# Kernel optimization log

Measured on AMD Instinct MI355X. Metric: run time of the kernel, lower is better.

The kernel has to match this reference:

```python
import jax, jax.numpy as jnp
import numpy as np

N = 50000          # nodes
E = 1_600_000      # edges (avg degree 32)
IN = 128           # in_channels
H1, C1 = 4, 8      # conv1: heads=4, out=8 -> concat 32
OUT = 64           # out_channels (conv2, heads=1)
NEG_SLOPE = 0.2    # PyG GATConv default LeakyReLU slope


def _gat_layer(x, edge_index, W, att_src, att_dst, bias, heads, out_ch):
    """PyG-style GATConv (concat=True, add_self_loops=True).
    x: [N, F_in], edge_index: [2, E], W: [F_in, heads*out_ch],
    att_src/att_dst: [heads, out_ch], bias: [heads*out_ch].
    """
    n = x.shape[0]
    loops = jnp.arange(n)
    src = jnp.concatenate([edge_index[0], loops])  # message source j
    dst = jnp.concatenate([edge_index[1], loops])  # aggregation target i

    h = (x @ W).reshape(n, heads, out_ch)                 # [N, H, C]
    a_src = jnp.sum(h * att_src, axis=-1)                 # [N, H]
    a_dst = jnp.sum(h * att_dst, axis=-1)                 # [N, H]

    logits = jax.nn.leaky_relu(a_src[src] + a_dst[dst], NEG_SLOPE)  # [E', H]
    # segment softmax over incoming edges of each destination node
    m = jax.ops.segment_max(logits, dst, num_segments=n)            # [N, H]
    e = jnp.exp(logits - m[dst])
    s = jax.ops.segment_sum(e, dst, num_segments=n)                 # [N, H]
    alpha = e / (s[dst] + 1e-16)                                    # [E', H]

    msg = h[src] * alpha[..., None]                                 # [E', H, C]
    out = jax.ops.segment_sum(msg, dst, num_segments=n)             # [N, H, C]
    return out.reshape(n, heads * out_ch) + bias


def setup_inputs() -> dict:
    key = jax.random.key(0)
    ks = jax.random.split(key, 10)
    g = 0.1
    x = jax.random.normal(ks[0], (N, IN), jnp.float32)
    edge_index = jax.random.randint(ks[1], (2, E), 0, N, dtype=jnp.int64)
    W1 = jax.random.normal(ks[2], (IN, H1 * C1), jnp.float32) * g
    att_src1 = jax.random.normal(ks[3], (H1, C1), jnp.float32) * g
    att_dst1 = jax.random.normal(ks[4], (H1, C1), jnp.float32) * g
    b1 = jnp.zeros((H1 * C1,), jnp.float32)
    W2 = jax.random.normal(ks[5], (H1 * C1, OUT), jnp.float32) * g
    att_src2 = jax.random.normal(ks[6], (1, OUT), jnp.float32) * g
    att_dst2 = jax.random.normal(ks[7], (1, OUT), jnp.float32) * g
    b2 = jnp.zeros((OUT,), jnp.float32)
    return {"x": x, "edge_index": edge_index,
            "W1": W1, "att_src1": att_src1, "att_dst1": att_dst1, "b1": b1,
            "W2": W2, "att_src2": att_src2, "att_dst2": att_dst2, "b2": b2}


def reference(x, edge_index, W1, att_src1, att_dst1, b1, W2, att_src2, att_dst2, b2):
    h = _gat_layer(x, edge_index, W1, att_src1, att_dst1, b1, H1, C1)   # [N, 32]
    h = jax.nn.relu(h)
    out = _gat_layer(h, edge_index, W2, att_src2, att_dst2, b2, 1, OUT)  # [N, 64]
    return out
```

## Files before the change

### kernel.cpp

```cpp
#include <hip/hip_runtime.h>
#include <hip/hip_bf16.h>

#define IN_CH 128
#define H1C1  32
#define NH1   4
#define OUTC  64
#define NEG   0.2f
#define RPAD  16
#define BSH   6
#define BSZ   64
#define NBMAX 1024
#define CHUNK 4096
#define CAP   3072
#define PCAP  4096

typedef __hip_bfloat16 bf16;
typedef unsigned int u32;
typedef unsigned short u16;

__device__ __forceinline__ u16 f2bf_bits(float f) {
  bf16 v = __float2bfloat16(f);
  return *(u16*)&v;
}
__device__ __forceinline__ float bflo(u32 g) { return __uint_as_float(g << 16); }
__device__ __forceinline__ float bfhi(u32 g) { return __uint_as_float(g & 0xFFFF0000u); }

__global__ __launch_bounds__(256) void k_bin_tr(
    const int* __restrict__ ei, int* __restrict__ bucket_fill,
    u32* __restrict__ data, int E, int n, int nb, int nA,
    const float* __restrict__ x, const float* __restrict__ W1,
    const float* __restrict__ as1, const float* __restrict__ ad1,
    u16* __restrict__ h1b, float* __restrict__ a_src, float* __restrict__ a_dst) {
  __shared__ __align__(16) char smem[28672];
  int t = threadIdx.x;
  if ((int)blockIdx.x < nA) {
    int* cnt   = (int*)smem;
    int* lbase = cnt + NBMAX;
    int* gbase = lbase + NBMAX;
    u32* staged = (u32*)(gbase + NBMAX);
    int lane = t & 63, wid = t >> 6;
    for (int b = t; b < nb; b += 256) cnt[b] = 0;
    __syncthreads();
    long base = (long)blockIdx.x * CHUNK;
    long totE = (long)E + n;
    u32 pk[CHUNK / 256];
    int bk[CHUNK / 256];
#pragma unroll
    for (int i = 0; i < CHUNK / 256; i++) {
      long e = base + i * 256 + t;
      if (e < totE) {
        int j, d;
        if (e < E) {
          j = ei[e]; d = ei[E + e];
          j = j < 0 ? 0 : (j >= n ? n - 1 : j);
          d = d < 0 ? 0 : (d >= n ? n - 1 : d);
        } else { j = d = (int)(e - E); }
        bk[i] = d >> BSH;
        pk[i] = ((u32)d << 16) | (u32)j;
        atomicAdd(&cnt[bk[i]], 1);
      } else bk[i] = -1;
    }
    __syncthreads();
    if (wid == 0) {
      int carry = 0;
      for (int b0 = 0; b0 < nb; b0 += 64) {
        int i = b0 + lane;
        int v = (i < nb) ? cnt[i] : 0;
        int orig = v;
        for (int off = 1; off < 64; off <<= 1) {
          int u = __shfl_up(v, off, 64);
          if (lane >= off) v += u;
        }
        if (i < nb) lbase[i] = carry + v - orig;
        carry += __shfl(v, 63, 64);
      }
    }
    __syncthreads();
    for (int b = t; b < nb; b += 256) {
      int c = cnt[b];
      gbase[b] = c ? atomicAdd(&bucket_fill[b], c) : 0;
      cnt[b] = 0;
    }
    __syncthreads();
#pragma unroll
    for (int i = 0; i < CHUNK / 256; i++) {
      if (bk[i] >= 0) {
        int loc = atomicAdd(&cnt[bk[i]], 1);
        staged[lbase[bk[i]] + loc] = pk[i];
      }
    }
    __syncthreads();
    long remL = totE - base;
    int rem = remL > CHUNK ? CHUNK : (int)remL;
    for (int idx = t; idx < rem; idx += 256) {
      u32 p = staged[idx];
      int b = (int)(p >> 16) >> BSH;
      int off2 = gbase[b] + (idx - lbase[b]);
      if (off2 < CAP) data[(size_t)b * CAP + off2] = p;
    }
  } else {
    float* W1s = (float*)smem;
    float* xs  = W1s + 32 * 128;
    for (int idx = t; idx < IN_CH * H1C1; idx += 256) {
      int k = idx >> 5, m = idx & 31;
      W1s[(k >> 2) * 128 + m * 4 + (k & 3)] = W1[idx];
    }
    int base = (blockIdx.x - nA) * 8;
    for (int idx = t; idx < 8 * IN_CH; idx += 256) {
      int row = idx >> 7, k = idx & 127;
      int nb2 = base + row;
      xs[idx] = (nb2 < n) ? x[(size_t)nb2 * IN_CH + k] : 0.f;
    }
    __syncthreads();
    int nl = t >> 5, m = t & 31;
    int node = base + nl;
    float acc = 0.f;
#pragma unroll
    for (int kg = 0; kg < 32; kg++) {
      float4 xv = *(const float4*)(xs + nl * IN_CH + kg * 4);
      float4 wv = *(const float4*)(W1s + kg * 128 + m * 4);
      acc += xv.x * wv.x + xv.y * wv.y + xv.z * wv.z + xv.w * wv.w;
    }
    float vs = acc * as1[m];
    float vd = acc * ad1[m];
    for (int off = 1; off < 8; off <<= 1) {
      vs += __shfl_xor(vs, off, 64);
      vd += __shfl_xor(vd, off, 64);
    }
    if (node < n) {
      h1b[node * H1C1 + m] = f2bf_bits(acc);
      if ((m & 7) == 0) {
        a_src[node * NH1 + (m >> 3)] = vs;
        a_dst[node * NH1 + (m >> 3)] = vd;
      }
    }
    if ((int)blockIdx.x == nA) {
      if (t < H1C1) h1b[n * H1C1 + t] = 0;
      if (t < NH1)  a_src[n * NH1 + t] = -1e30f;
    }
  }
}

__global__ __launch_bounds__(256) void k_bucket_scatter(
    const u32* __restrict__ data, const int* __restrict__ bucket_fill,
    int2* __restrict__ rowse, int* __restrict__ col, int n) {
  __shared__ int cur[BSZ];
  __shared__ int rp[BSZ];
  __shared__ int pd[BSZ];
  int t = threadIdx.x;
  int b = blockIdx.x;
  if (t < BSZ) cur[t] = 0;
  __syncthreads();
  int s = b * CAP;
  int cnt = bucket_fill[b];
  if (cnt > CAP) cnt = CAP;
  for (int i = t; i < cnt; i += 256)
    atomicAdd(&cur[(data[s + i] >> 16) & (BSZ - 1)], 1);
  __syncthreads();
  if (t < 64) {
    int raw = cur[t];
    int v = (raw + RPAD - 1) & ~(RPAD - 1);
    int orig = v;
    for (int off = 1; off < 64; off <<= 1) {
      int u = __shfl_up(v, off, 64);
      if (t >= off) v += u;
    }
    int r = b * PCAP + v - orig;
    rp[t] = r;
    pd[t] = orig;
    cur[t] = r;
    int node = (b << BSH) + t;
    if (node < n) rowse[node] = make_int2(r, r + orig);
  }
  __syncthreads();
  for (int i = t; i < cnt; i += 256) {
    u32 p = data[s + i];
    int dl = (int)(p >> 16) & (BSZ - 1);
    int pos = atomicAdd(&cur[dl], 1);
    col[pos] = (int)(p & 0xFFFFu);
  }
  __syncthreads();
  if (t < 64) {
    int c = cur[t];
    int end = rp[t] + pd[t];
    for (int k = c; k < end; k++) col[k] = n;
  }
}

__global__ __launch_bounds__(256) void k_l1_agg(
    const int2* __restrict__ rowse, const int* __restrict__ col,
    const u16* __restrict__ h1b, const float* __restrict__ a_src,
    const float* __restrict__ a_dst, const float* __restrict__ b1,
    const float* __restrict__ W2, const float* __restrict__ as2,
    const float* __restrict__ ad2,
    u16* __restrict__ h2, float* __restrict__ a_src2, float* __restrict__ a_dst2,
    int n) {
  __shared__ float W2s[8 * 256];
  __shared__ float hsh[16][H1C1];
  __shared__ int   js[4][64];
  __shared__ float wsh[4][NH1][68];
  int t = threadIdx.x;
  int wid = t >> 6, lane = t & 63;
  {
    int c = t & 63;
#pragma unroll
    for (int g = 0; g < 2; g++) {
      int kg = (t >> 6) + 4 * g;
      float4 v;
      v.x = W2[(kg * 4 + 0) * OUTC + c];
      v.y = W2[(kg * 4 + 1) * OUTC + c];
      v.z = W2[(kg * 4 + 2) * OUTC + c];
      v.w = W2[(kg * 4 + 3) * OUTC + c];
      *(float4*)(W2s + kg * 256 + c * 4) = v;
    }
  }
  int o = lane >> 3, u = lane & 7;
  int hd = u >> 1;
  for (int s = 0; s < 4; s++) {
    int node = blockIdx.x * 16 + wid * 4 + s;
    if (node >= n) continue;
    int2 se = rowse[node];
    int rs = se.x, re = se.y;
    float4 ad = *(const float4*)(a_dst + node * NH1);
    float a0 = 0.f, a1 = 0.f, a2 = 0.f, a3 = 0.f, sw = 0.f;
    for (int tb = rs; tb < re; tb += 64) {
      int kmax = re - tb; if (kmax > 64) kmax = 64;
      if (lane < kmax) {
        int j = col[tb + lane];
        float4 as = *(const float4*)(a_src + j * NH1);
        float l0 = as.x + ad.x; l0 = l0 > 0.f ? l0 : NEG * l0;
        float l1 = as.y + ad.y; l1 = l1 > 0.f ? l1 : NEG * l1;
        float l2 = as.z + ad.z; l2 = l2 > 0.f ? l2 : NEG * l2;
        float l3 = as.w + ad.w; l3 = l3 > 0.f ? l3 : NEG * l3;
        js[wid][lane] = j;
        wsh[wid][0][lane] = __expf(l0);
        wsh[wid][1][lane] = __expf(l1);
        wsh[wid][2][lane] = __expf(l2);
        wsh[wid][3][lane] = __expf(l3);
      }
      for (int k = 0; k < kmax; k += 16) {
        int j0 = js[wid][k + o];
        int j1 = js[wid][k + 8 + o];
        float w0 = wsh[wid][hd][k + o];
        float w1 = wsh[wid][hd][k + 8 + o];
        uint2 g0 = *(const uint2*)(h1b + j0 * H1C1 + 4 * u);
        uint2 g1 = *(const uint2*)(h1b + j1 * H1C1 + 4 * u);
        a0 += w0 * bflo(g0.x) + w1 * bflo(g1.x);
        a1 += w0 * bfhi(g0.x) + w1 * bfhi(g1.x);
        a2 += w0 * bflo(g0.y) + w1 * bflo(g1.y);
        a3 += w0 * bfhi(g0.y) + w1 * bfhi(g1.y);
        sw += w0 + w1;
      }
    }
    for (int off = 8; off < 64; off <<= 1) {
      a0 += __shfl_xor(a0, off, 64);
      a1 += __shfl_xor(a1, off, 64);
      a2 += __shfl_xor(a2, off, 64);
      a3 += __shfl_xor(a3, off, 64);
      sw += __shfl_xor(sw, off, 64);
    }
    if (o == 0) {
      float inv = 1.f / (sw + 1e-16f);
      int c = 4 * u;
      hsh[wid * 4 + s][c]     = fmaxf(a0 * inv + b1[c], 0.f);
      hsh[wid * 4 + s][c + 1] = fmaxf(a1 * inv + b1[c + 1], 0.f);
      hsh[wid * 4 + s][c + 2] = fmaxf(a2 * inv + b1[c + 2], 0.f);
      hsh[wid * 4 + s][c + 3] = fmaxf(a3 * inv + b1[c + 3], 0.f);
    }
  }
  __syncthreads();
  float as2l = as2[lane], ad2l = ad2[lane];
  for (int r = 0; r < 4; r++) {
    int nl = wid * 4 + r;
    int node = blockIdx.x * 16 + nl;
    float acc = 0.f;
#pragma unroll
    for (int kg = 0; kg < 8; kg++) {
      float4 hv = *(const float4*)(&hsh[nl][kg * 4]);
      float4 wv = *(const float4*)(W2s + kg * 256 + lane * 4);
      acc += hv.x * wv.x + hv.y * wv.y + hv.z * wv.z + hv.w * wv.w;
    }
    float vs = acc * as2l;
    float vd = acc * ad2l;
    for (int off = 1; off < 64; off <<= 1) {
      vs += __shfl_xor(vs, off, 64);
      vd += __shfl_xor(vd, off, 64);
    }
    if (node < n) {
      h2[node * OUTC + lane] = f2bf_bits(acc);
      if (lane == 0) { a_src2[node] = vs; a_dst2[node] = vd; }
    }
  }
  if (blockIdx.x == 0) {
    if (t < OUTC) h2[n * OUTC + t] = 0;
    if (t == 0)   a_src2[n] = -1e30f;
  }
}

__global__ __launch_bounds__(256) void k_l2_agg(
    const int2* __restrict__ rowse, const int* __restrict__ col,
    const u16* __restrict__ h2, const float* __restrict__ a_src2,
    const float* __restrict__ a_dst2, const float* __restrict__ b2v,
    float* __restrict__ out, int n) {
  __shared__ int   js[4][64];
  __shared__ float wsh[4][64];
  int t = threadIdx.x;
  int wid = t >> 6, lane = t & 63;
  int o = lane >> 4, u = lane & 15;
  for (int s = 0; s < 4; s++) {
    int node = blockIdx.x * 16 + wid * 4 + s;
    if (node >= n) continue;
    int2 se = rowse[node];
    int rs = se.x, re = se.y;
    float ad = a_dst2[node];
    float a0 = 0.f, a1 = 0.f, a2 = 0.f, a3 = 0.f, sw = 0.f;
    for (int tb = rs; tb < re; tb += 64) {
      int kmax = re - tb; if (kmax > 64) kmax = 64;
      if (lane < kmax) {
        int j = col[tb + lane];
        float lg = a_src2[j] + ad;
        lg = lg > 0.f ? lg : NEG * lg;
        js[wid][lane] = j;
        wsh[wid][lane] = __expf(lg);
      }
      for (int k = 0; k < kmax; k += 16) {
        int j0 = js[wid][k + o];
        int j1 = js[wid][k + 4 + o];
        int j2 = js[wid][k + 8 + o];
        int j3 = js[wid][k + 12 + o];
        float w0 = wsh[wid][k + o];
        float w1 = wsh[wid][k + 4 + o];
        float w2 = wsh[wid][k + 8 + o];
        float w3 = wsh[wid][k + 12 + o];
        uint2 g0 = *(const uint2*)(h2 + j0 * OUTC + 4 * u);
        uint2 g1 = *(const uint2*)(h2 + j1 * OUTC + 4 * u);
        uint2 g2 = *(const uint2*)(h2 + j2 * OUTC + 4 * u);
        uint2 g3 = *(const uint2*)(h2 + j3 * OUTC + 4 * u);
        a0 += w0 * bflo(g0.x) + w1 * bflo(g1.x);
        a0 += w2 * bflo(g2.x) + w3 * bflo(g3.x);
        a1 += w0 * bfhi(g0.x) + w1 * bfhi(g1.x);
        a1 += w2 * bfhi(g2.x) + w3 * bfhi(g3.x);
        a2 += w0 * bflo(g0.y) + w1 * bflo(g1.y);
        a2 += w2 * bflo(g2.y) + w3 * bflo(g3.y);
        a3 += w0 * bfhi(g0.y) + w1 * bfhi(g1.y);
        a3 += w2 * bfhi(g2.y) + w3 * bfhi(g3.y);
        sw += (w0 + w1) + (w2 + w3);
      }
    }
    for (int off = 16; off < 64; off <<= 1) {
      a0 += __shfl_xor(a0, off, 64);
      a1 += __shfl_xor(a1, off, 64);
      a2 += __shfl_xor(a2, off, 64);
      a3 += __shfl_xor(a3, off, 64);
      sw += __shfl_xor(sw, off, 64);
    }
    if (o == 0) {
      float inv = 1.f / (sw + 1e-16f);
      int c = 4 * u;
      float4 ov;
      ov.x = a0 * inv + b2v[c];
      ov.y = a1 * inv + b2v[c + 1];
      ov.z = a2 * inv + b2v[c + 2];
      ov.w = a3 * inv + b2v[c + 3];
      *(float4*)(out + node * OUTC + c) = ov;
    }
  }
}


extern "C" void kernel_launch(void* const* d_in, const int* in_sizes, int n_in,
                              void* d_out, int out_size, void* d_ws, size_t ws_size,
                              hipStream_t stream) {
  const float* x   = (const float*)d_in[0];
  const int*   ei  = (const int*)d_in[1];
  const float* W1  = (const float*)d_in[2];
  const float* as1 = (const float*)d_in[3];
  const float* ad1 = (const float*)d_in[4];
  const float* b1  = (const float*)d_in[5];
  const float* W2  = (const float*)d_in[6];
  const float* as2 = (const float*)d_in[7];
  const float* ad2 = (const float*)d_in[8];
  const float* b2  = (const float*)d_in[9];
  float* out = (float*)d_out;

  int n = in_sizes[0] / IN_CH;
  int E = in_sizes[1] / 2;
  int nb = (n + BSZ - 1) >> BSH;
  long tot = (long)E + n;
  int nA = (int)((tot + CHUNK - 1) / CHUNK);
  int nTr = (n + 7) / 8;

  char* w = (char*)d_ws;
  auto al = [](size_t v) { return (v + 255) & ~(size_t)255; };
  size_t off = 0;
  int*  bucket_fill = (int*)(w + off);  off += al((size_t)nb * 4);
  int2* rowse       = (int2*)(w + off); off += al((size_t)(n + 1) * 8);
  u32*  data        = (u32*)(w + off);  off += al((size_t)nb * CAP * 4);
  int*  col         = (int*)(w + off);  off += al((size_t)nb * PCAP * 4);
  u16*  h1b         = (u16*)(w + off);  off += al((size_t)(n + 1) * H1C1 * 2);
  float* a_src1     = (float*)(w + off); off += al((size_t)(n + 1) * NH1 * 4);
  float* a_dst1     = (float*)(w + off); off += al((size_t)(n + 1) * NH1 * 4);
  u16*  h2          = (u16*)(w + off);  off += al((size_t)(n + 1) * OUTC * 2);
  float* a_src2     = (float*)(w + off); off += al((size_t)(n + 1) * 4);
  float* a_dst2     = (float*)(w + off); off += al((size_t)(n + 1) * 4);

  hipMemsetAsync(bucket_fill, 0, (size_t)nb * 4, stream);
  hipLaunchKernelGGL(k_bin_tr, dim3(nA + nTr), dim3(256), 0, stream,
                     ei, bucket_fill, data, E, n, nb, nA,
                     x, W1, as1, ad1, h1b, a_src1, a_dst1);
  hipLaunchKernelGGL(k_bucket_scatter, dim3(nb), dim3(256), 0, stream,
                     data, bucket_fill, rowse, col, n);

  hipLaunchKernelGGL(k_l1_agg, dim3((n + 15) / 16), dim3(256), 0, stream,
                     rowse, col, h1b, a_src1, a_dst1, b1,
                     W2, as2, ad2, h2, a_src2, a_dst2, n);

  hipLaunchKernelGGL(k_l2_agg, dim3((n + 15) / 16), dim3(256), 0, stream,
                     rowse, col, h2, a_src2, a_dst2, b2, out, n);
}
```

Baseline: 212.3 us.

## Keep W1 in registers and process 32 nodes per transform block

The feature-transform blocks of the binning kernel now hold a K-slice of W1 in registers, loaded straight from global memory, and no longer stage the whole weight matrix in shared memory. Each block handles 32 nodes instead of 8, with K split across lane groups and reduced by cross-lane shuffles. Stores to h1b are packed bf16 pairs. The aim is to cut the repeated per-block W1 staging cost and the block count, at the price of more registers and shuffle work.

```diff
diff --git a/kernel.cpp b/kernel.cpp
--- a/kernel.cpp
+++ b/kernel.cpp
@@ -13,6 +13,7 @@
 #define CHUNK 4096
 #define CAP   3072
 #define PCAP  4096
+#define NPB   32
 
 typedef __hip_bfloat16 bf16;
 typedef unsigned int u32;
@@ -99,39 +100,67 @@
       if (off2 < CAP) data[(size_t)b * CAP + off2] = p;
     }
   } else {
-    float* W1s = (float*)smem;
-    float* xs  = W1s + 32 * 128;
-    for (int idx = t; idx < IN_CH * H1C1; idx += 256) {
-      int k = idx >> 5, m = idx & 31;
-      W1s[(k >> 2) * 128 + m * 4 + (k & 3)] = W1[idx];
-    }
-    int base = (blockIdx.x - nA) * 8;
-    for (int idx = t; idx < 8 * IN_CH; idx += 256) {
-      int row = idx >> 7, k = idx & 127;
-      int nb2 = base + row;
-      xs[idx] = (nb2 < n) ? x[(size_t)nb2 * IN_CH + k] : 0.f;
-    }
-    __syncthreads();
-    int nl = t >> 5, m = t & 31;
-    int node = base + nl;
-    float acc = 0.f;
-#pragma unroll
-    for (int kg = 0; kg < 32; kg++) {
-      float4 xv = *(const float4*)(xs + nl * IN_CH + kg * 4);
-      float4 wv = *(const float4*)(W1s + kg * 128 + m * 4);
-      acc += xv.x * wv.x + xv.y * wv.y + xv.z * wv.z + xv.w * wv.w;
-    }
-    float vs = acc * as1[m];
-    float vd = acc * ad1[m];
-    for (int off = 1; off < 8; off <<= 1) {
-      vs += __shfl_xor(vs, off, 64);
-      vd += __shfl_xor(vd, off, 64);
-    }
-    if (node < n) {
-      h1b[node * H1C1 + m] = f2bf_bits(acc);
-      if ((m & 7) == 0) {
-        a_src[node * NH1 + (m >> 3)] = vs;
-        a_dst[node * NH1 + (m >> 3)] = vd;
+    float* xs = (float*)smem;
+    int base = ((int)blockIdx.x - nA) * NPB;
+    for (int i4 = t; i4 < NPB * 32; i4 += 256) {
+      int nd = base + (i4 >> 5);
+      float4 v = make_float4(0.f, 0.f, 0.f, 0.f);
+      if (nd < n) v = ((const float4*)x)[(size_t)base * 32 + i4];
+      ((float4*)xs)[i4] = v;
+    }
+    int mg = t & 7, ks = (t >> 3) & 7, ns = t >> 6;
+    int m0 = mg * 4;
+    float4 w[4][4];
+#pragma unroll
+    for (int kk = 0; kk < 4; kk++) {
+      int q = (kk + ks) & 3;
+      int k0 = ks * 16 + q * 4;
+      float4 t0 = *(const float4*)(W1 + (k0 + 0) * H1C1 + m0);
+      float4 t1 = *(const float4*)(W1 + (k0 + 1) * H1C1 + m0);
+      float4 t2 = *(const float4*)(W1 + (k0 + 2) * H1C1 + m0);
+      float4 t3 = *(const float4*)(W1 + (k0 + 3) * H1C1 + m0);
+      w[kk][0] = make_float4(t0.x, t1.x, t2.x, t3.x);
+      w[kk][1] = make_float4(t0.y, t1.y, t2.y, t3.y);
+      w[kk][2] = make_float4(t0.z, t1.z, t2.z, t3.z);
+      w[kk][3] = make_float4(t0.w, t1.w, t2.w, t3.w);
+    }
+    float4 asq = *(const float4*)(as1 + m0);
+    float4 adq = *(const float4*)(ad1 + m0);
+    __syncthreads();
+#pragma unroll 2
+    for (int r = 0; r < 8; r++) {
+      int nl = r * 4 + ns;
+      const float4* xrow = (const float4*)(xs + nl * IN_CH + ks * 16);
+      float a0 = 0.f, a1 = 0.f, a2 = 0.f, a3 = 0.f;
+#pragma unroll
+      for (int kk = 0; kk < 4; kk++) {
+        int q = (kk + ks) & 3;
+        float4 xv = xrow[q];
+        a0 += xv.x * w[kk][0].x + xv.y * w[kk][0].y + xv.z * w[kk][0].z + xv.w * w[kk][0].w;
+        a1 += xv.x * w[kk][1].x + xv.y * w[kk][1].y + xv.z * w[kk][1].z + xv.w * w[kk][1].w;
+        a2 += xv.x * w[kk][2].x + xv.y * w[kk][2].y + xv.z * w[kk][2].z + xv.w * w[kk][2].w;
+        a3 += xv.x * w[kk][3].x + xv.y * w[kk][3].y + xv.z * w[kk][3].z + xv.w * w[kk][3].w;
+      }
+#pragma unroll
+      for (int off = 8; off < 64; off <<= 1) {
+        a0 += __shfl_xor(a0, off, 64);
+        a1 += __shfl_xor(a1, off, 64);
+        a2 += __shfl_xor(a2, off, 64);
+        a3 += __shfl_xor(a3, off, 64);
+      }
+      int node = base + nl;
+      if (ks == 0 && node < n) {
+        float vs = a0 * asq.x + a1 * asq.y + a2 * asq.z + a3 * asq.w;
+        float vd = a0 * adq.x + a1 * adq.y + a2 * adq.z + a3 * adq.w;
+        vs += __shfl_xor(vs, 1, 64);
+        vd += __shfl_xor(vd, 1, 64);
+        u32 lo = (u32)f2bf_bits(a0) | ((u32)f2bf_bits(a1) << 16);
+        u32 hi = (u32)f2bf_bits(a2) | ((u32)f2bf_bits(a3) << 16);
+        *(uint2*)(h1b + (size_t)node * H1C1 + m0) = make_uint2(lo, hi);
+        if ((mg & 1) == 0) {
+          a_src[node * NH1 + (mg >> 1)] = vs;
+          a_dst[node * NH1 + (mg >> 1)] = vd;
+        }
       }
     }
     if ((int)blockIdx.x == nA) {
@@ -388,7 +417,7 @@
   int nb = (n + BSZ - 1) >> BSH;
   long tot = (long)E + n;
   int nA = (int)((tot + CHUNK - 1) / CHUNK);
-  int nTr = (n + 7) / 8;
+  int nTr = (n + NPB - 1) / NPB;
 
   char* w = (char*)d_ws;
   auto al = [](size_t v) { return (v + 255) & ~(size_t)255; };
```

Result: faster. 205.7 us (-3.1%).
